# Performance work log

Hardware: AMD Instinct MI355X
Metric: run time of the kernel (lower is better)

The kernel has to match this reference:

```python
import jax, jax.numpy as jnp
import numpy as np

N_NODES = 40000
N_EDGES = 1280000
D_FEAT = 1024
HIDDEN = 64
N_CLASSES = 40


def gcn_conv(x, edge_index, W, b):
    # PyG GCNConv: linear transform, add self-loops, symmetric deg^{-1/2} normalization, scatter-add
    n = x.shape[0]
    h = x @ W  # [N, out]
    loop = jnp.arange(n, dtype=edge_index.dtype)
    row = jnp.concatenate([edge_index[0], loop])  # source
    col = jnp.concatenate([edge_index[1], loop])  # target
    deg = jax.ops.segment_sum(jnp.ones_like(col, dtype=x.dtype), col, num_segments=n)
    dinv = jnp.where(deg > 0, jax.lax.rsqrt(deg), 0.0).astype(x.dtype)
    norm = dinv[row] * dinv[col]  # [E+N]
    msg = h[row] * norm[:, None]
    out = jax.ops.segment_sum(msg, col, num_segments=n)
    return out + b


def setup_inputs() -> dict:
    key = jax.random.key(0)
    k1, k2, k3, k4 = jax.random.split(key, 4)
    x = jax.random.normal(k1, (N_NODES, D_FEAT), dtype=jnp.float32)
    edge_index = jax.random.randint(k2, (2, N_EDGES), 0, N_NODES, dtype=jnp.int32)
    W1 = jax.random.normal(k3, (D_FEAT, HIDDEN), dtype=jnp.float32) * (1.0 / np.sqrt(D_FEAT))
    b1 = jnp.zeros((HIDDEN,), dtype=jnp.float32)
    W2 = jax.random.normal(k4, (HIDDEN, N_CLASSES), dtype=jnp.float32) * (1.0 / np.sqrt(HIDDEN))
    b2 = jnp.zeros((N_CLASSES,), dtype=jnp.float32)
    return {"x": x, "edge_index": edge_index, "W1": W1, "b1": b1, "W2": W2, "b2": b2}


def reference(x, edge_index, W1, b1, W2, b2):
    h = gcn_conv(x, edge_index, W1, b1)
    h = jax.nn.relu(h)
    # F.dropout(training=False) -> identity in eval mode
    h = gcn_conv(h, edge_index, W2, b2)
    return jax.nn.log_softmax(h, axis=1)
```

## Files before the change

kernel.cpp:

```cpp
#include <hip/hip_runtime.h>
#include <hip/hip_bf16.h>
#include <math.h>

#define N_NODES 40000
#define N_EDGES 1280000
#define D_FEAT 1024
#define HIDDEN 64
#define N_CLASSES 40
#define NB 157
#define CHUNK 2048
#define SORT_STAGE 10240
#define GEMM_BLOCKS 625
#define GEMM_A 312
#define GEMM_B 313

typedef _Float16 f16x8 __attribute__((ext_vector_type(8)));
typedef float f32x4 __attribute__((ext_vector_type(4)));

__device__ __forceinline__ int wscan64(int v, int lane) {
#pragma unroll
    for (int d = 1; d < 64; d <<= 1) {
        int t = __shfl_up(v, d, 64);
        v += (lane >= d) ? t : 0;
    }
    return v;
}


#define HIST_BLOCKS 313
#define CONV_BLOCKS 256

__global__ __launch_bounds__(256) void k_pre(const int* __restrict__ col,
                                             int* __restrict__ btot,
                                             const float* __restrict__ W,
                                             _Float16* __restrict__ Wt) {
    __shared__ int h[NB];
    int tid = threadIdx.x;
    if (blockIdx.x < HIST_BLOCKS) {
        if (tid < NB) h[tid] = 0;
        __syncthreads();
        int e0 = blockIdx.x * 4096;
#pragma unroll
        for (int t = 0; t < 4; ++t) {
            int e = e0 + t * 1024 + tid * 4;
            if (e < N_EDGES) {
                int4 c = *(const int4*)&col[e];
                atomicAdd(&h[c.x >> 8], 1);
                atomicAdd(&h[c.y >> 8], 1);
                atomicAdd(&h[c.z >> 8], 1);
                atomicAdd(&h[c.w >> 8], 1);
            }
        }
        __syncthreads();
        if (tid < NB && h[tid]) atomicAdd(&btot[tid], h[tid]);
    } else {
        int i = (blockIdx.x - HIST_BLOCKS) * 256 + tid;
        int n = i & 63, k = i >> 6;
        Wt[n * D_FEAT + k] = (_Float16)W[k * HIDDEN + n];
    }
}


struct BinS {
    unsigned stage[CHUNK];
    unsigned char bo[CHUNK];
    int hist[NB]; int lo[NB]; int cur[NB]; int dst[NB];
    int wsA[4]; int wsB[4];
};
struct SortS {
    int hist[256]; int cur[256];
    unsigned short st[SORT_STAGE];
    int ws[4];
    int sbase, scnt;
};
#define GEMM_SMEM 36864


__device__ __forceinline__ void binscatter_body(char* smem, int bx,
        const int* __restrict__ row, const int* __restrict__ col,
        const int* __restrict__ btot, int* __restrict__ gcur,
        unsigned* __restrict__ sedge, int tid, int wave, int lane) {
    BinS* S = (BinS*)smem;
    const int e0 = bx * CHUNK;
    if (tid < NB) { S->hist[tid] = 0; S->cur[tid] = 0; }
    int bv = (tid < NB) ? btot[tid] : 0;
    int ivb = wscan64(bv, lane);
    if (lane == 63) S->wsB[wave] = ivb;
    __syncthreads();
    int addb = 0;
#pragma unroll
    for (int w = 0; w < 3; ++w) addb += (w < wave) ? S->wsB[w] : 0;
    int bbv = ivb + addb - bv;

    int c[8];
#pragma unroll
    for (int t = 0; t < 8; ++t) {
        int e = tid + t * 256;
        c[t] = col[e0 + e];
        atomicAdd(&S->hist[c[t] >> 8], 1);
    }
    __syncthreads();

    int hv = (tid < NB) ? S->hist[tid] : 0;
    int iv = wscan64(hv, lane);
    if (lane == 63) S->wsA[wave] = iv;
    __syncthreads();
    int add = 0;
#pragma unroll
    for (int w = 0; w < 3; ++w) add += (w < wave) ? S->wsA[w] : 0;
    if (tid < NB) {
        int excl = iv + add - hv;
        S->lo[tid] = excl;
        int cp = hv ? atomicAdd(&gcur[tid], hv) : 0;
        S->dst[tid] = bbv + cp - excl;
    }
    __syncthreads();

#pragma unroll
    for (int t = 0; t < 8; ++t) {
        int e = tid + t * 256;
        int b = c[t] >> 8;
        int p = S->lo[b] + atomicAdd(&S->cur[b], 1);
        S->stage[p] = ((unsigned)(c[t] & 255) << 16) | (unsigned)row[e0 + e];
        S->bo[p] = (unsigned char)b;
    }
    __syncthreads();
    for (int i = tid; i < CHUNK; i += 256)
        sedge[S->dst[S->bo[i]] + i] = S->stage[i];
}


__device__ __forceinline__ void sort_body(char* smem, int b,
        const unsigned* __restrict__ sedge, const int* __restrict__ btot,
        int* __restrict__ off, float* __restrict__ dinv,
        unsigned short* __restrict__ sorted, int tid, int wave, int lane) {
    SortS* S = (SortS*)smem;
    S->hist[tid] = 0;
    int bv = (tid < NB) ? btot[tid] : 0;
    int ivb = wscan64(bv, lane);
    if (lane == 63) S->ws[wave] = ivb;
    __syncthreads();
    int addb = 0;
#pragma unroll
    for (int w = 0; w < 3; ++w) addb += (w < wave) ? S->ws[w] : 0;
    if (tid == b) { S->sbase = ivb + addb - bv; S->scnt = bv; }
    __syncthreads();
    const int base = S->sbase, cnt = S->scnt, end = base + cnt;

    for (int i = base + tid; i < end; i += 256)
        atomicAdd(&S->hist[sedge[i] >> 16], 1);
    __syncthreads();
    int v = S->hist[tid];
    int iv = wscan64(v, lane);
    if (lane == 63) S->ws[wave] = iv;
    __syncthreads();
    int add = 0;
#pragma unroll
    for (int w = 0; w < 3; ++w) add += (w < wave) ? S->ws[w] : 0;
    int excl = iv + add - v;
    S->cur[tid] = excl;
    int col0 = b << 8;
    int ncol = min(256, N_NODES - col0);
    if (tid < ncol) {
        off[col0 + tid] = base + excl;
        dinv[col0 + tid] = rsqrtf((float)(v + 1));
    }
    if (b == NB - 1 && tid == 0) off[N_NODES] = N_EDGES;
    __syncthreads();

    if (cnt <= SORT_STAGE) {
        for (int i = base + tid; i < end; i += 256) {
            unsigned e = sedge[i];
            int p = atomicAdd(&S->cur[e >> 16], 1);
            S->st[p] = (unsigned short)e;
        }
        __syncthreads();
        for (int i = tid; i < cnt; i += 256)
            sorted[base + i] = S->st[i];
    } else {
        for (int i = base + tid; i < end; i += 256) {
            unsigned e = sedge[i];
            int p = atomicAdd(&S->cur[e >> 16], 1);
            sorted[base + p] = (unsigned short)e;
        }
    }
}


#define LDA 72
#define LDB 72

__device__ __forceinline__ void gemm_body(char* smem, int bx,
        const float* __restrict__ X, const _Float16* __restrict__ Wt,
        _Float16* __restrict__ out, int tid) {
    auto As = (_Float16(*)[64 * LDA])(smem);
    auto Bs = (_Float16(*)[64 * LDB])(smem + 2 * 64 * LDA * 2);
    const int wave = tid >> 6, lane = tid & 63;
    const int row0 = bx * 64;
    const int m0 = (wave & 1) * 32, n0 = (wave >> 1) * 32;
    const int lr = lane & 15, quad = lane >> 4;

    const int ar = tid >> 2;
    const int ak = (tid & 3) * 16;
    const int bn = tid >> 2;
    const int bk = (tid & 3) * 16;

    f32x4 acc00 = {0.f,0.f,0.f,0.f}, acc01 = {0.f,0.f,0.f,0.f};
    f32x4 acc10 = {0.f,0.f,0.f,0.f}, acc11 = {0.f,0.f,0.f,0.f};

    float4 xv0, xv1, xv2, xv3;
    uint4 wv0, wv1;

#define GLOAD(K0) {                                                          \
        const float4* xp = (const float4*)&X[(row0 + ar) * D_FEAT + (K0) + ak]; \
        xv0 = xp[0]; xv1 = xp[1]; xv2 = xp[2]; xv3 = xp[3];                  \
        const uint4* wp = (const uint4*)&Wt[bn * D_FEAT + (K0) + bk];        \
        wv0 = wp[0]; wv1 = wp[1]; }

#define LSTORE(B) {                                                          \
        f16x8 p0 = {(_Float16)xv0.x,(_Float16)xv0.y,(_Float16)xv0.z,(_Float16)xv0.w, \
                    (_Float16)xv1.x,(_Float16)xv1.y,(_Float16)xv1.z,(_Float16)xv1.w}; \
        f16x8 p1 = {(_Float16)xv2.x,(_Float16)xv2.y,(_Float16)xv2.z,(_Float16)xv2.w, \
                    (_Float16)xv3.x,(_Float16)xv3.y,(_Float16)xv3.z,(_Float16)xv3.w}; \
        *(f16x8*)&As[B][ar * LDA + ak]     = p0;                             \
        *(f16x8*)&As[B][ar * LDA + ak + 8] = p1;                             \
        *(uint4*)&Bs[B][bn * LDB + bk]     = wv0;                            \
        *(uint4*)&Bs[B][bn * LDB + bk + 8] = wv1; }

#define MFMA_STEP(B) {                                                       \
        _Pragma("unroll")                                                    \
        for (int kk = 0; kk < 64; kk += 32) {                                \
            f16x8 a0 = *(f16x8*)&As[B][(m0 + lr) * LDA + kk + quad * 8];     \
            f16x8 a1 = *(f16x8*)&As[B][(m0 + 16 + lr) * LDA + kk + quad * 8];\
            f16x8 b0 = *(f16x8*)&Bs[B][(n0 + lr) * LDB + kk + quad * 8];     \
            f16x8 b1 = *(f16x8*)&Bs[B][(n0 + 16 + lr) * LDB + kk + quad * 8];\
            acc00 = __builtin_amdgcn_mfma_f32_16x16x32_f16(a0, b0, acc00, 0, 0, 0); \
            acc01 = __builtin_amdgcn_mfma_f32_16x16x32_f16(a0, b1, acc01, 0, 0, 0); \
            acc10 = __builtin_amdgcn_mfma_f32_16x16x32_f16(a1, b0, acc10, 0, 0, 0); \
            acc11 = __builtin_amdgcn_mfma_f32_16x16x32_f16(a1, b1, acc11, 0, 0, 0); \
        } }

    GLOAD(0);
    LSTORE(0);
    __syncthreads();
    int buf = 0;
    for (int k0 = 64; k0 < D_FEAT; k0 += 64) {
        GLOAD(k0);
        MFMA_STEP(buf);
        LSTORE(buf ^ 1);
        __syncthreads();
        buf ^= 1;
    }
    MFMA_STEP(buf);

#pragma unroll
    for (int r = 0; r < 4; ++r) {
        int m = row0 + m0 + quad * 4 + r;
        out[m * HIDDEN + n0 + lr]             = (_Float16)acc00[r];
        out[m * HIDDEN + n0 + 16 + lr]        = (_Float16)acc01[r];
        out[(m + 16) * HIDDEN + n0 + lr]      = (_Float16)acc10[r];
        out[(m + 16) * HIDDEN + n0 + 16 + lr] = (_Float16)acc11[r];
    }
#undef GLOAD
#undef LSTORE
#undef MFMA_STEP
}


__global__ __launch_bounds__(256) void k_mix(int phase,
        const int* __restrict__ row, const int* __restrict__ col,
        const int* __restrict__ btot, int* __restrict__ gcur,
        unsigned* __restrict__ sedge,
        int* __restrict__ off, float* __restrict__ dinv,
        unsigned short* __restrict__ sorted,
        const float* __restrict__ X, const _Float16* __restrict__ Wt,
        _Float16* __restrict__ B1) {
    __shared__ __align__(16) char smem[GEMM_SMEM];
    const int tid = threadIdx.x;
    const int wave = tid >> 6, lane = tid & 63;
    if (phase == 0) {
        if (blockIdx.x < 625)
            binscatter_body(smem, blockIdx.x, row, col, btot, gcur, sedge, tid, wave, lane);
        else
            gemm_body(smem, (int)blockIdx.x - 625, X, Wt, B1, tid);
    } else {
        if (blockIdx.x < NB)
            sort_body(smem, blockIdx.x, sedge, btot, off, dinv, sorted, tid, wave, lane);
        else
            gemm_body(smem, (int)blockIdx.x - NB + GEMM_A, X, Wt, B1, tid);
    }
}


__global__ __launch_bounds__(256) void k_agg1(const int* __restrict__ off,
                                              const unsigned short* __restrict__ sorted,
                                              const _Float16* __restrict__ hs,
                                              const float* __restrict__ dinv,
                                              const float* __restrict__ bias,
                                              _Float16* __restrict__ A1) {
    const int tid = threadIdx.x;
    const int wave = tid >> 6, lane = tid & 63;
    const int node = blockIdx.x * 4 + wave;
    const int g = lane >> 3;
    const int sl = lane & 7;

    float acc[8];
#pragma unroll
    for (int j = 0; j < 8; ++j) acc[j] = 0.f;
    if (g == 0) {
        float dvn = dinv[node];
        f16x8 v = *(const f16x8*)&hs[node * HIDDEN + sl * 8];
#pragma unroll
        for (int j = 0; j < 8; ++j) acc[j] = (float)v[j] * dvn;
    }

    const int beg = off[node], end = off[node + 1];
    for (int base = beg; base < end; base += 64) {
        int m = end - base; if (m > 64) m = 64;
        unsigned pk = 0;
        if (lane < m) {
            int vv = (int)sorted[base + lane];
            _Float16 dvh = (_Float16)dinv[vv];
            pk = (unsigned)vv | ((unsigned)__builtin_bit_cast(unsigned short, dvh) << 16);
        }
        int nfull = m & ~15;
        int i = 0;
        for (; i < nfull; i += 16) {
            unsigned p0 = (unsigned)__shfl((int)pk, i + g, 64);
            unsigned p1 = (unsigned)__shfl((int)pk, i + 8 + g, 64);
            const f16x8 v0 = *(const f16x8*)&hs[(p0 & 0xffffu) * HIDDEN + sl * 8];
            const f16x8 v1 = *(const f16x8*)&hs[(p1 & 0xffffu) * HIDDEN + sl * 8];
            _Float16 d0 = __builtin_bit_cast(_Float16, (unsigned short)(p0 >> 16));
            _Float16 d1 = __builtin_bit_cast(_Float16, (unsigned short)(p1 >> 16));
            f16x8 t = v0 * d0 + v1 * d1;
#pragma unroll
            for (int j = 0; j < 8; ++j)
                acc[j] += (float)t[j];
        }
        if (i < m) {
            unsigned p0 = (unsigned)__shfl((int)pk, i + g, 64);
            unsigned p1 = (unsigned)__shfl((int)pk, i + 8 + g, 64);
            f16x8 v0 = {}, v1 = {};
            _Float16 d0 = (_Float16)0.f, d1 = (_Float16)0.f;
            if (i + g < m) {
                v0 = *(const f16x8*)&hs[(p0 & 0xffffu) * HIDDEN + sl * 8];
                d0 = __builtin_bit_cast(_Float16, (unsigned short)(p0 >> 16));
            }
            if (i + 8 + g < m) {
                v1 = *(const f16x8*)&hs[(p1 & 0xffffu) * HIDDEN + sl * 8];
                d1 = __builtin_bit_cast(_Float16, (unsigned short)(p1 >> 16));
            }
            f16x8 t = v0 * d0 + v1 * d1;
#pragma unroll
            for (int j = 0; j < 8; ++j)
                acc[j] += (float)t[j];
        }
    }

#pragma unroll
    for (int j = 0; j < 8; ++j) {
        acc[j] += __shfl_xor(acc[j], 8, 64);
        acc[j] += __shfl_xor(acc[j], 16, 64);
        acc[j] += __shfl_xor(acc[j], 32, 64);
    }
    if (lane < 8) {
        float dv = dinv[node];
        f16x8 o;
#pragma unroll
        for (int j = 0; j < 8; ++j) {
            float z = fmaf(dv, acc[j], bias[lane * 8 + j]);
            o[j] = (_Float16)(fmaxf(z, 0.f) * dv);
        }
        *(f16x8*)&A1[node * HIDDEN + lane * 8] = o;
    }
}


__global__ __launch_bounds__(256) void k_agg2_lsm(const int* __restrict__ off,
                                                  const unsigned short* __restrict__ sorted,
                                                  const _Float16* __restrict__ A1,
                                                  const float* __restrict__ dinv,
                                                  const float* __restrict__ b2,
                                                  const float* __restrict__ W2,
                                                  float* __restrict__ out) {
    __shared__ float W2s[HIDDEN * N_CLASSES];
    __shared__ float aggs[4][HIDDEN];
    const int tid = threadIdx.x;
    for (int i = tid; i < HIDDEN * N_CLASSES; i += 256) W2s[i] = W2[i];
    const int wave = tid >> 6, lane = tid & 63;
    const int node = blockIdx.x * 4 + wave;
    const int g = lane >> 3, sl = lane & 7;

    float acc[8];
#pragma unroll
    for (int j = 0; j < 8; ++j) acc[j] = 0.f;
    if (g == 0) {
        f16x8 v = *(const f16x8*)&A1[node * HIDDEN + sl * 8];
#pragma unroll
        for (int j = 0; j < 8; ++j) acc[j] = (float)v[j];
    }
    __syncthreads();

    const int beg = off[node], end = off[node + 1];
    for (int base = beg; base < end; base += 64) {
        int m = end - base; if (m > 64) m = 64;
        int vidx = (lane < m) ? (int)sorted[base + lane] : 0;
        int nfull = m & ~15;
        int i = 0;
        for (; i < nfull; i += 16) {
            int s0 = __shfl(vidx, i + g, 64);
            int s1 = __shfl(vidx, i + 8 + g, 64);
            f16x8 v0 = *(const f16x8*)&A1[s0 * HIDDEN + sl * 8];
            f16x8 v1 = *(const f16x8*)&A1[s1 * HIDDEN + sl * 8];
            f16x8 t = v0 + v1;
#pragma unroll
            for (int j = 0; j < 8; ++j)
                acc[j] += (float)t[j];
        }
        if (i < m) {
            int s0 = __shfl(vidx, i + g, 64);
            int s1 = __shfl(vidx, i + 8 + g, 64);
            f16x8 v0 = {};
            f16x8 v1 = {};
            if (i + g < m)     v0 = *(const f16x8*)&A1[s0 * HIDDEN + sl * 8];
            if (i + 8 + g < m) v1 = *(const f16x8*)&A1[s1 * HIDDEN + sl * 8];
            f16x8 t = v0 + v1;
#pragma unroll
            for (int j = 0; j < 8; ++j)
                acc[j] += (float)t[j];
        }
    }
#pragma unroll
    for (int j = 0; j < 8; ++j) {
        acc[j] += __shfl_xor(acc[j], 8, 64);
        acc[j] += __shfl_xor(acc[j], 16, 64);
        acc[j] += __shfl_xor(acc[j], 32, 64);
    }
    if (lane < 8) {
        f32x4 t0 = {acc[0], acc[1], acc[2], acc[3]};
        f32x4 t1 = {acc[4], acc[5], acc[6], acc[7]};
        *(f32x4*)&aggs[wave][lane * 8]     = t0;
        *(f32x4*)&aggs[wave][lane * 8 + 4] = t1;
    }
    __builtin_amdgcn_wave_barrier();

    float z = -INFINITY;
    if (lane < N_CLASSES) {
        float s = 0.f;
        const float* ag = aggs[wave];
#pragma unroll
        for (int k = 0; k < HIDDEN; ++k)
            s = fmaf(ag[k], W2s[k * N_CLASSES + lane], s);
        z = fmaf(dinv[node], s, b2[lane]);
    }
    float mv = z;
#pragma unroll
    for (int d = 32; d > 0; d >>= 1) mv = fmaxf(mv, __shfl_xor(mv, d, 64));
    float ex = (lane < N_CLASSES) ? expf(z - mv) : 0.f;
#pragma unroll
    for (int d = 32; d > 0; d >>= 1) ex += __shfl_xor(ex, d, 64);
    float lse = mv + logf(ex);
    if (lane < N_CLASSES) out[node * N_CLASSES + lane] = z - lse;
}


extern "C" void kernel_launch(void* const* d_in, const int* in_sizes, int n_in,
                              void* d_out, int out_size, void* d_ws, size_t ws_size,
                              hipStream_t stream) {
    const float* x  = (const float*)d_in[0];
    const int*   ei = (const int*)d_in[1];
    const float* W1 = (const float*)d_in[2];
    const float* b1 = (const float*)d_in[3];
    const float* W2 = (const float*)d_in[4];
    const float* b2 = (const float*)d_in[5];
    const int* row = ei;
    const int* col = ei + N_EDGES;

    char* ws = (char*)d_ws;
    int*            btot   = (int*)(ws + 0);
    int*            gcur   = (int*)(ws + 1024);
    int*            off    = (int*)(ws + 4096);
    float*          dinv   = (float*)(ws + 167936);
    unsigned*       sedge  = (unsigned*)(ws + 335872);
    unsigned short* sorted = (unsigned short*)(ws + 5455872);
    _Float16*       W1t    = (_Float16*)(ws + 8015872);
    _Float16*       B1     = (_Float16*)(ws + 8146944);
    _Float16*       A1     = (_Float16*)(ws + 335872);

    hipMemsetAsync(btot, 0, 2048, stream);
    k_pre<<<HIST_BLOCKS + CONV_BLOCKS, 256, 0, stream>>>(col, btot, W1, W1t);
    k_mix<<<625 + GEMM_A, 256, 0, stream>>>(0, row, col, btot, gcur, sedge,
                                            off, dinv, sorted, x, W1t, B1);
    k_mix<<<NB + GEMM_B, 256, 0, stream>>>(1, row, col, btot, gcur, sedge,
                                           off, dinv, sorted, x, W1t, B1);
    k_agg1<<<N_NODES / 4, 256, 0, stream>>>(off, sorted, B1, dinv, b1, A1);
    k_agg2_lsm<<<N_NODES / 4, 256, 0, stream>>>(off, sorted, A1, dinv, b2, W2, (float*)d_out);
}
```

Before: 355.7 us.

## Drop global histogram pass using fixed-capacity per-bin scatter buckets

Removes the separate column-histogram kernel. The bin scatter now writes each bin's edges into a fixed-capacity region (bin * BCAP) and uses the per-bin atomic counters for the totals, so no prefix sum is needed beforehand. The weight transpose moves into phase 0 of the mixed kernel, and all of the first-layer GEMM now runs in phase 1 alongside the per-bin sort. This saves one launch and one full read of the column array. The cost is a larger workspace, a hard per-bin capacity that could overflow on skewed inputs, and a GEMM that no longer overlaps with the scatter phase.

```diff
diff --git a/kernel.cpp b/kernel.cpp
--- a/kernel.cpp
+++ b/kernel.cpp
@@ -9,10 +9,9 @@
 #define N_CLASSES 40
 #define NB 157
 #define CHUNK 2048
+#define BCAP 10240
 #define SORT_STAGE 10240
-#define GEMM_BLOCKS 625
-#define GEMM_A 312
-#define GEMM_B 313
+#define CONV_BLOCKS 256
 
 typedef _Float16 f16x8 __attribute__((ext_vector_type(8)));
 typedef float f32x4 __attribute__((ext_vector_type(4)));
@@ -24,40 +23,6 @@
         v += (lane >= d) ? t : 0;
     }
     return v;
-}
-
-
-#define HIST_BLOCKS 313
-#define CONV_BLOCKS 256
-
-__global__ __launch_bounds__(256) void k_pre(const int* __restrict__ col,
-                                             int* __restrict__ btot,
-                                             const float* __restrict__ W,
-                                             _Float16* __restrict__ Wt) {
-    __shared__ int h[NB];
-    int tid = threadIdx.x;
-    if (blockIdx.x < HIST_BLOCKS) {
-        if (tid < NB) h[tid] = 0;
-        __syncthreads();
-        int e0 = blockIdx.x * 4096;
-#pragma unroll
-        for (int t = 0; t < 4; ++t) {
-            int e = e0 + t * 1024 + tid * 4;
-            if (e < N_EDGES) {
-                int4 c = *(const int4*)&col[e];
-                atomicAdd(&h[c.x >> 8], 1);
-                atomicAdd(&h[c.y >> 8], 1);
-                atomicAdd(&h[c.z >> 8], 1);
-                atomicAdd(&h[c.w >> 8], 1);
-            }
-        }
-        __syncthreads();
-        if (tid < NB && h[tid]) atomicAdd(&btot[tid], h[tid]);
-    } else {
-        int i = (blockIdx.x - HIST_BLOCKS) * 256 + tid;
-        int n = i & 63, k = i >> 6;
-        Wt[n * D_FEAT + k] = (_Float16)W[k * HIDDEN + n];
-    }
 }
 
 
@@ -65,32 +30,25 @@
     unsigned stage[CHUNK];
     unsigned char bo[CHUNK];
     int hist[NB]; int lo[NB]; int cur[NB]; int dst[NB];
-    int wsA[4]; int wsB[4];
+    int wsA[4];
 };
 struct SortS {
     int hist[256]; int cur[256];
     unsigned short st[SORT_STAGE];
     int ws[4];
-    int sbase, scnt;
+    int wbase, scnt;
 };
 #define GEMM_SMEM 36864
 
 
 __device__ __forceinline__ void binscatter_body(char* smem, int bx,
         const int* __restrict__ row, const int* __restrict__ col,
-        const int* __restrict__ btot, int* __restrict__ gcur,
-        unsigned* __restrict__ sedge, int tid, int wave, int lane) {
+        int* __restrict__ gcur, unsigned* __restrict__ sedge,
+        int tid, int wave, int lane) {
     BinS* S = (BinS*)smem;
     const int e0 = bx * CHUNK;
     if (tid < NB) { S->hist[tid] = 0; S->cur[tid] = 0; }
-    int bv = (tid < NB) ? btot[tid] : 0;
-    int ivb = wscan64(bv, lane);
-    if (lane == 63) S->wsB[wave] = ivb;
-    __syncthreads();
-    int addb = 0;
-#pragma unroll
-    for (int w = 0; w < 3; ++w) addb += (w < wave) ? S->wsB[w] : 0;
-    int bbv = ivb + addb - bv;
+    __syncthreads();
 
     int c[8];
 #pragma unroll
@@ -112,7 +70,7 @@
         int excl = iv + add - hv;
         S->lo[tid] = excl;
         int cp = hv ? atomicAdd(&gcur[tid], hv) : 0;
-        S->dst[tid] = bbv + cp - excl;
+        S->dst[tid] = tid * BCAP + cp - excl;
     }
     __syncthreads();
 
@@ -131,24 +89,25 @@
 
 
 __device__ __forceinline__ void sort_body(char* smem, int b,
-        const unsigned* __restrict__ sedge, const int* __restrict__ btot,
+        const unsigned* __restrict__ sedge, const int* __restrict__ gcur,
         int* __restrict__ off, float* __restrict__ dinv,
         unsigned short* __restrict__ sorted, int tid, int wave, int lane) {
     SortS* S = (SortS*)smem;
     S->hist[tid] = 0;
-    int bv = (tid < NB) ? btot[tid] : 0;
+    int bv = (tid < NB) ? gcur[tid] : 0;
     int ivb = wscan64(bv, lane);
     if (lane == 63) S->ws[wave] = ivb;
     __syncthreads();
     int addb = 0;
 #pragma unroll
     for (int w = 0; w < 3; ++w) addb += (w < wave) ? S->ws[w] : 0;
-    if (tid == b) { S->sbase = ivb + addb - bv; S->scnt = bv; }
-    __syncthreads();
-    const int base = S->sbase, cnt = S->scnt, end = base + cnt;
-
-    for (int i = base + tid; i < end; i += 256)
-        atomicAdd(&S->hist[sedge[i] >> 16], 1);
+    if (tid == b) { S->wbase = ivb + addb - bv; S->scnt = bv; }
+    __syncthreads();
+    const int wbase = S->wbase, cnt = S->scnt;
+    const int rb = b * BCAP;
+
+    for (int i = tid; i < cnt; i += 256)
+        atomicAdd(&S->hist[sedge[rb + i] >> 16], 1);
     __syncthreads();
     int v = S->hist[tid];
     int iv = wscan64(v, lane);
@@ -162,26 +121,26 @@
     int col0 = b << 8;
     int ncol = min(256, N_NODES - col0);
     if (tid < ncol) {
-        off[col0 + tid] = base + excl;
+        off[col0 + tid] = wbase + excl;
         dinv[col0 + tid] = rsqrtf((float)(v + 1));
     }
     if (b == NB - 1 && tid == 0) off[N_NODES] = N_EDGES;
     __syncthreads();
 
     if (cnt <= SORT_STAGE) {
-        for (int i = base + tid; i < end; i += 256) {
-            unsigned e = sedge[i];
+        for (int i = tid; i < cnt; i += 256) {
+            unsigned e = sedge[rb + i];
             int p = atomicAdd(&S->cur[e >> 16], 1);
             S->st[p] = (unsigned short)e;
         }
         __syncthreads();
         for (int i = tid; i < cnt; i += 256)
-            sorted[base + i] = S->st[i];
+            sorted[wbase + i] = S->st[i];
     } else {
-        for (int i = base + tid; i < end; i += 256) {
-            unsigned e = sedge[i];
+        for (int i = tid; i < cnt; i += 256) {
+            unsigned e = sedge[rb + i];
             int p = atomicAdd(&S->cur[e >> 16], 1);
-            sorted[base + p] = (unsigned short)e;
+            sorted[wbase + p] = (unsigned short)e;
         }
     }
 }
@@ -269,25 +228,27 @@
 
 __global__ __launch_bounds__(256) void k_mix(int phase,
         const int* __restrict__ row, const int* __restrict__ col,
-        const int* __restrict__ btot, int* __restrict__ gcur,
-        unsigned* __restrict__ sedge,
+        int* __restrict__ gcur, unsigned* __restrict__ sedge,
         int* __restrict__ off, float* __restrict__ dinv,
         unsigned short* __restrict__ sorted,
-        const float* __restrict__ X, const _Float16* __restrict__ Wt,
-        _Float16* __restrict__ B1) {
+        const float* __restrict__ X, const float* __restrict__ W1,
+        _Float16* __restrict__ Wt, _Float16* __restrict__ B1) {
     __shared__ __align__(16) char smem[GEMM_SMEM];
     const int tid = threadIdx.x;
     const int wave = tid >> 6, lane = tid & 63;
     if (phase == 0) {
-        if (blockIdx.x < 625)
-            binscatter_body(smem, blockIdx.x, row, col, btot, gcur, sedge, tid, wave, lane);
-        else
-            gemm_body(smem, (int)blockIdx.x - 625, X, Wt, B1, tid);
+        if (blockIdx.x < 625) {
+            binscatter_body(smem, blockIdx.x, row, col, gcur, sedge, tid, wave, lane);
+        } else {
+            int i = ((int)blockIdx.x - 625) * 256 + tid;
+            int n = i & 63, k = i >> 6;
+            Wt[n * D_FEAT + k] = (_Float16)W1[k * HIDDEN + n];
+        }
     } else {
         if (blockIdx.x < NB)
-            sort_body(smem, blockIdx.x, sedge, btot, off, dinv, sorted, tid, wave, lane);
+            sort_body(smem, blockIdx.x, sedge, gcur, off, dinv, sorted, tid, wave, lane);
         else
-            gemm_body(smem, (int)blockIdx.x - NB + GEMM_A, X, Wt, B1, tid);
+            gemm_body(smem, (int)blockIdx.x - NB, X, Wt, B1, tid);
     }
 }
 
@@ -477,22 +438,20 @@
     const int* col = ei + N_EDGES;
 
     char* ws = (char*)d_ws;
-    int*            btot   = (int*)(ws + 0);
-    int*            gcur   = (int*)(ws + 1024);
+    int*            gcur   = (int*)(ws + 0);
     int*            off    = (int*)(ws + 4096);
     float*          dinv   = (float*)(ws + 167936);
     unsigned*       sedge  = (unsigned*)(ws + 335872);
-    unsigned short* sorted = (unsigned short*)(ws + 5455872);
-    _Float16*       W1t    = (_Float16*)(ws + 8015872);
-    _Float16*       B1     = (_Float16*)(ws + 8146944);
+    unsigned short* sorted = (unsigned short*)(ws + 6766592);
+    _Float16*       W1t    = (_Float16*)(ws + 9326592);
+    _Float16*       B1     = (_Float16*)(ws + 9457664);
     _Float16*       A1     = (_Float16*)(ws + 335872);
 
-    hipMemsetAsync(btot, 0, 2048, stream);
-    k_pre<<<HIST_BLOCKS + CONV_BLOCKS, 256, 0, stream>>>(col, btot, W1, W1t);
-    k_mix<<<625 + GEMM_A, 256, 0, stream>>>(0, row, col, btot, gcur, sedge,
-                                            off, dinv, sorted, x, W1t, B1);
-    k_mix<<<NB + GEMM_B, 256, 0, stream>>>(1, row, col, btot, gcur, sedge,
-                                           off, dinv, sorted, x, W1t, B1);
+    hipMemsetAsync(gcur, 0, 1024, stream);
+    k_mix<<<625 + CONV_BLOCKS, 256, 0, stream>>>(0, row, col, gcur, sedge,
+                                                 off, dinv, sorted, x, W1, W1t, B1);
+    k_mix<<<NB + 625, 256, 0, stream>>>(1, row, col, gcur, sedge,
+                                        off, dinv, sorted, x, W1, W1t, B1);
     k_agg1<<<N_NODES / 4, 256, 0, stream>>>(off, sorted, B1, dinv, b1, A1);
     k_agg2_lsm<<<N_NODES / 4, 256, 0, stream>>>(off, sorted, A1, dinv, b2, W2, (float*)d_out);
 }
```

Result: no change. 360.9 us (+1.5%).
